# Kernel optimization log

Measured on AMD Instinct MI355X. Metric: run time of the kernel, lower is better.

## Reference

```python
import jax, jax.numpy as jnp
import numpy as np

N, G, MAX_N, E, H = 20000, 200, 100, 320000, 4
F_IN, NHID, NCLS = 128, 128, 10
DQ = 2 * NHID   # pooling-stack input dim = 2*nhid
K1 = 25         # ceil(0.25 * avg_num_nodes)


def _lin(key, fi, fo):
    kw, kb = jax.random.split(key)
    s = 1.0 / np.sqrt(fi)
    return (jax.random.uniform(kw, (fi, fo), jnp.float32, -s, s),
            jax.random.uniform(kb, (fo,), jnp.float32, -s, s))


def setup_inputs():
    key = jax.random.key(0)
    ks = jax.random.split(key, 32)
    x = jax.random.normal(ks[0], (N, F_IN), jnp.float32)
    gid = jax.random.randint(ks[1], (E,), 0, G)
    u = jax.random.randint(ks[2], (E,), 0, MAX_N)
    v = jax.random.randint(ks[3], (E,), 0, MAX_N)
    edge_index = jnp.stack([gid * MAX_N + u, gid * MAX_N + v]).astype(jnp.int32)
    batch = (jnp.arange(N) // MAX_N).astype(jnp.int32)
    d = {}
    d['x'], d['edge_index'], d['batch'] = x, edge_index, batch
    d['W1'], d['b1'] = _lin(ks[4], F_IN, NHID)
    d['W2'], d['b2'] = _lin(ks[5], NHID, NHID)
    d['S0'] = jax.random.normal(ks[6], (1, K1, DQ), jnp.float32) * (1.0 / np.sqrt(DQ))
    d['Wq0'], d['bq0'] = _lin(ks[7], DQ, DQ)
    d['Wk0'], d['bk0'] = _lin(ks[8], DQ, DQ)
    d['Wv0'], d['bv0'] = _lin(ks[9], DQ, DQ)
    d['Wo0'], d['bo0'] = _lin(ks[10], DQ, DQ)
    d['Wq1'], d['bq1'] = _lin(ks[11], DQ, NHID)
    d['Wk1'], d['bk1'] = _lin(ks[12], DQ, NHID)
    d['Wv1'], d['bv1'] = _lin(ks[13], DQ, NHID)
    d['Wo1'], d['bo1'] = _lin(ks[14], NHID, NHID)
    d['S2'] = jax.random.normal(ks[15], (1, 1, NHID), jnp.float32) * (1.0 / np.sqrt(NHID))
    d['Wq2'], d['bq2'] = _lin(ks[16], NHID, NHID)
    d['Wk2'], d['bk2'] = _lin(ks[17], NHID, NHID)
    d['Wv2'], d['bv2'] = _lin(ks[18], NHID, NHID)
    d['Wo2'], d['bo2'] = _lin(ks[19], NHID, NHID)
    d['Wl'], d['bl'] = _lin(ks[20], NHID, NHID)
    d['Wc1'], d['bc1'] = _lin(ks[21], NHID, NHID)
    d['Wc2'], d['bc2'] = _lin(ks[22], NHID, NHID // 2)
    d['Wc3'], d['bc3'] = _lin(ks[23], NHID // 2, NCLS)
    return d


def gcn(h, src, dst, W, b):
    # PyG GCNConv: add self loops, sym-normalize, scatter-add, bias
    h = h @ W
    loop = jnp.arange(N, dtype=src.dtype)
    s = jnp.concatenate([src, loop])
    t = jnp.concatenate([dst, loop])
    deg = jax.ops.segment_sum(jnp.ones(s.shape[0], h.dtype), t, num_segments=N)
    dinv = jax.lax.rsqrt(jnp.maximum(deg, 1.0))
    norm = (dinv[s] * dinv[t])[:, None]
    return jax.ops.segment_sum(h[s] * norm, t, num_segments=N) + b


def to_dense(v, batch):
    counts = jax.ops.segment_sum(jnp.ones(v.shape[0], jnp.int32), batch, num_segments=G)
    start = jnp.cumsum(counts) - counts
    pos = jnp.arange(v.shape[0]) - start[batch]
    dense = jnp.zeros((G, MAX_N, v.shape[1]), v.dtype).at[batch, pos].set(v)
    mask = jnp.zeros((G, MAX_N), bool).at[batch, pos].set(True)
    return dense, mask


def attn_block(Q, K, V, Wo, bo, mask_bias):
    # MAB core with cluster=True: softmax over the QUERY (seed) axis, ln=False
    B, nq, dv = Q.shape
    dh = dv // H
    Qh = Q.reshape(B, nq, H, dh)
    Kh = K.reshape(B, K.shape[1], H, dh)
    Vh = V.reshape(B, V.shape[1], H, dh)
    score = jnp.einsum('bqhd,bkhd->bhqk', Qh, Kh) / jnp.sqrt(jnp.float32(dv))
    if mask_bias is not None:
        score = score + mask_bias[:, None, None, :]
    A = jax.nn.softmax(score, axis=2)  # cluster assignment over seeds
    O = Q + jnp.einsum('bhqk,bkhd->bqhd', A, Vh).reshape(B, nq, dv)
    return O + jax.nn.relu(O @ Wo + bo)


def reference(x, edge_index, batch, W1, b1, W2, b2, S0, Wq0, bq0, Wk0, bk0, Wv0, bv0, Wo0, bo0,
              Wq1, bq1, Wk1, bk1, Wv1, bv1, Wo1, bo1, S2, Wq2, bq2, Wk2, bk2, Wv2, bv2, Wo2, bo2,
              Wl, bl, Wc1, bc1, Wc2, bc2, Wc3, bc3):
    src, dst = edge_index[0], edge_index[1]
    x1 = jax.nn.relu(gcn(x, src, dst, W1, b1))
    x2 = jax.nn.relu(gcn(x1, src, dst, W2, b2))
    p1 = jax.ops.segment_sum(x1, batch, num_segments=G)  # global_add_pool
    p2 = jax.ops.segment_sum(x2, batch, num_segments=G)
    xcat = jnp.concatenate([x1, x2], axis=1)             # [N, 2*nhid]
    dense, mask = to_dense(xcat, batch)
    mask_bias = (1.0 - mask.astype(jnp.float32)) * -1e9
    # --- GMPool_G: PMA with GCNConv for K/V on the node graph ---
    Kd, _ = to_dense(gcn(xcat, src, dst, Wk0, bk0), batch)
    Vd, _ = to_dense(gcn(xcat, src, dst, Wv0, bv0), batch)
    Q0 = jnp.broadcast_to(S0, (G, K1, DQ)) @ Wq0 + bq0
    O0 = attn_block(Q0, Kd, Vd, Wo0, bo0, mask_bias)     # [G, 25, 256]
    # --- SelfAtt (SAB), mask consumed above ---
    Q1 = O0 @ Wq1 + bq1
    K1d = O0 @ Wk1 + bk1
    V1d = O0 @ Wv1 + bv1
    O1 = attn_block(Q1, K1d, V1d, Wo1, bo1, None)        # [G, 25, 128]
    # --- GMPool_I: PMA with 1 seed ---
    Q2 = jnp.broadcast_to(S2, (G, 1, NHID)) @ Wq2 + bq2
    K2d = O1 @ Wk2 + bk2
    V2d = O1 @ Wv2 + bv2
    O2 = attn_block(Q2, K2d, V2d, Wo2, bo2, None)        # [G, 1, 128]
    z = (O2 @ Wl + bl)[:, 0, :]
    z = jax.nn.relu(z @ Wc1 + bc1)                        # dropout = identity at eval
    z = jax.nn.relu(z @ Wc2 + bc2)
    logits = z @ Wc3 + bc3
    return (logits, p1, p2)
```

## Files before the change

### kernel.cpp

```cpp
#include <hip/hip_runtime.h>
#include <hip/hip_bf16.h>
#include <cstdint>
#include <cstddef>

typedef __hip_bfloat16 bf16;
typedef __attribute__((ext_vector_type(8))) short s16x8;
typedef __attribute__((ext_vector_type(4))) float f32x4;

#define MAXN 100
#define HH   4
#define FIN  128
#define KS1  25

static inline int ceil_div(int a, int b){ return (a + b - 1) / b; }

__device__ inline short f2bf(float f){
  unsigned int u = __float_as_uint(f);
  u = (u + 0x7FFF + ((u >> 16) & 1)) >> 16;
  return (short)u;
}
__device__ inline float loadf(const void* s, int i, bool isbf){
  return isbf ? __bfloat162float(((const bf16*)s)[i]) : ((const float*)s)[i];
}
__device__ inline bool block_sniff(const void* x, int tid, int* flagS){
  if (tid < 64){
    unsigned short b = ((const unsigned short*)x)[2 * tid];
    float v = __uint_as_float(((unsigned)b) << 16);
    float a = fabsf(v);
    bool ok = (a >= 6.1e-5f && a <= 16384.f);
    unsigned long long m = __ballot(ok);
    if (tid == 0) *flagS = (__popcll(m) >= 32) ? 1 : 0;
  }
  __syncthreads();
  return *flagS != 0;
}

struct PrepBatch {
  const void* src[40];
  void*       dst[40];
  int         a[40];
  int         b[40];
  int         blk0[41];
  int         ne;
  const void* xptr;
};

__global__ __launch_bounds__(256) void prep_all(PrepBatch pb){
  __shared__ int flagS;
  int tid = threadIdx.x;
  bool isbf = block_sniff(pb.xptr, tid, &flagS);
  int blk = blockIdx.x;
  int t = 0;
  while (t + 1 < pb.ne && pb.blk0[t + 1] <= blk) t++;
  int local = blk - pb.blk0[t];
  const void* s = pb.src[t];
  int bt = pb.b[t];
  if (bt < 0){
    float val = (bt == -2) ? 1.0f : 0.0f;
    int n = pb.a[t];
    float* d = (float*)pb.dst[t];
    int v = local * 256 + tid;
    int base = v * 4;
    if (base + 3 < n) ((float4*)d)[v] = make_float4(val, val, val, val);
    else for (int j = base; j < n && j < base + 4; j++) d[j] = val;
  } else if (bt == 0){
    int n = pb.a[t];
    float* d = (float*)pb.dst[t];
    int v = local * 256 + tid;
    int base = v * 4;
    if (base + 3 < n){
      float4 f;
      if (isbf){
        ushort4 u = ((const ushort4*)s)[v];
        f.x = __uint_as_float(((unsigned)u.x) << 16);
        f.y = __uint_as_float(((unsigned)u.y) << 16);
        f.z = __uint_as_float(((unsigned)u.z) << 16);
        f.w = __uint_as_float(((unsigned)u.w) << 16);
      } else f = ((const float4*)s)[v];
      ((float4*)d)[v] = f;
    } else {
      for (int j = base; j < n && j < base + 4; j++) d[j] = loadf(s, j, isbf);
    }
  } else {
    int K = pb.a[t], Nn = bt, ldt = K + 8;
    short* d = (short*)pb.dst[t];
    int i = local * 256 + tid;
    if (i < K * Nn){
      int n = i / K, k = i - n * K;
      d[(size_t)n * ldt + k] = f2bf(loadf(s, (size_t)k * Nn + n, isbf));
    }
  }
}

__global__ __launch_bounds__(256) void adj_cnt(const int* __restrict__ src, const int* __restrict__ dst,
                                               float* __restrict__ A, int e){
  int i = blockIdx.x * 256 + threadIdx.x;
  if (i >= e) return;
  int s = src[i], d = dst[i];
  int g = d / MAXN;
  int dl = d - g * MAXN;
  int sl = s - (s / MAXN) * MAXN;
  atomicAdd(&A[(size_t)g * (MAXN * MAXN) + dl * MAXN + sl], 1.0f);
}

#define GLDK 136
__global__ __launch_bounds__(512) void gcn_all(
    const void* __restrict__ X,
    const float* __restrict__ Adj,
    const short* __restrict__ W1t, const float* __restrict__ b1,
    const short* __restrict__ W2t, const float* __restrict__ b2,
    short* __restrict__ xaggB,
    float* __restrict__ p1, float* __restrict__ p2)
{
  __shared__ short As[112 * GLDK];
  __shared__ short S1[112 * GLDK];
  __shared__ short S2[128 * GLDK];
  __shared__ short S4[128 * GLDK];
  __shared__ float dinvL[112];
  __shared__ int flagS;
  int g = blockIdx.x;
  int tid = threadIdx.x;
  bool isbf = block_sniff(X, tid, &flagS);
  int wave = tid >> 6, lane = tid & 63;
  int quad = lane >> 4, l16 = lane & 15;
  int gn = wave * 16 + l16;

  for (int i = tid; i < 112 * GLDK / 2; i += 512){ ((int*)As)[i] = 0; ((int*)S1)[i] = 0; }
  for (int i = tid; i < 128 * GLDK / 2; i += 512){ ((int*)S2)[i] = 0; ((int*)S4)[i] = 0; }

  const float* Ag = Adj + (size_t)g * (MAXN * MAXN);
  if (tid < 400){
    int r = tid >> 2, j0 = (tid & 3) * 25;
    const float* row = Ag + r * MAXN + j0;
    float s = 0.f;
#pragma unroll
    for (int j = 0; j < 25; j++) s += row[j];
    s += __shfl_xor(s, 1); s += __shfl_xor(s, 2);
    if ((tid & 3) == 0) dinvL[r] = rsqrtf(1.0f + s);
  }
  __syncthreads();

  for (int i = tid; i < MAXN * MAXN; i += 512){
    int r = i / MAXN, s = i - r * MAXN;
    float v = Ag[i] + (r == s ? 1.0f : 0.0f);
    As[r * GLDK + s] = f2bf(v * dinvL[r] * dinvL[s]);
  }
  for (int i = tid; i < MAXN * 16; i += 512){
    int r = i >> 4, k8 = (i & 15) << 3;
    s16x8 v;
    if (isbf){
      v = *reinterpret_cast<const s16x8*>((const short*)X + (size_t)(g * MAXN + r) * 128 + k8);
    } else {
      const float* ap = (const float*)X + (size_t)(g * MAXN + r) * 128 + k8;
      float4 f0 = *reinterpret_cast<const float4*>(ap);
      float4 f1 = *reinterpret_cast<const float4*>(ap + 4);
      v[0] = f2bf(f0.x); v[1] = f2bf(f0.y); v[2] = f2bf(f0.z); v[3] = f2bf(f0.w);
      v[4] = f2bf(f1.x); v[5] = f2bf(f1.y); v[6] = f2bf(f1.z); v[7] = f2bf(f1.w);
    }
    *reinterpret_cast<s16x8*>(&S1[r * GLDK + k8]) = v;
  }
  __syncthreads();

  f32x4 acc[7];
  auto zacc = [&](){
#pragma unroll
    for (int rt = 0; rt < 7; rt++) acc[rt] = (f32x4){0.f,0.f,0.f,0.f};
  };
  auto passL = [&](const short* Abuf, const short* Bbuf){
#pragma unroll
    for (int kt = 0; kt < 4; kt++){
      int kb = kt * 32 + quad * 8;
      s16x8 bf0 = *reinterpret_cast<const s16x8*>(&Bbuf[gn * GLDK + kb]);
#pragma unroll
      for (int rt = 0; rt < 7; rt++){
        s16x8 a = *reinterpret_cast<const s16x8*>(&Abuf[(rt * 16 + l16) * GLDK + kb]);
        acc[rt] = __builtin_amdgcn_mfma_f32_16x16x32_bf16(a, bf0, acc[rt], 0, 0, 0);
      }
    }
  };
  auto passG = [&](const short* Abuf, const short* __restrict__ Bt){
#pragma unroll
    for (int kt = 0; kt < 4; kt++){
      int kb = kt * 32 + quad * 8;
      s16x8 bf0 = *reinterpret_cast<const s16x8*>(&Bt[(size_t)gn * 136 + kb]);
#pragma unroll
      for (int rt = 0; rt < 7; rt++){
        s16x8 a = *reinterpret_cast<const s16x8*>(&Abuf[(rt * 16 + l16) * GLDK + kb]);
        acc[rt] = __builtin_amdgcn_mfma_f32_16x16x32_bf16(a, bf0, acc[rt], 0, 0, 0);
      }
    }
  };
  auto writeB = [&](short* Bbuf){
#pragma unroll
    for (int rt = 0; rt < 7; rt++){
      short4 o;
      o.x = f2bf(acc[rt][0]); o.y = f2bf(acc[rt][1]);
      o.z = f2bf(acc[rt][2]); o.w = f2bf(acc[rt][3]);
      *reinterpret_cast<short4*>(&Bbuf[gn * GLDK + rt * 16 + quad * 4]) = o;
    }
  };

  float s1sum = 0.f, s2sum = 0.f;
  auto hopEpi = [&](const float* bias, short* AoutA, short* BoutB, float& sum){
    float bv = bias[gn];
#pragma unroll
    for (int rt = 0; rt < 7; rt++){
      float vals[4];
#pragma unroll
      for (int r = 0; r < 4; r++){
        int row = rt * 16 + quad * 4 + r;
        float v = fmaxf(acc[rt][r] + bv, 0.f);
        vals[r] = v;
        if (row < MAXN) sum += v;
      }
      short4 o;
      o.x = f2bf(vals[0]); o.y = f2bf(vals[1]); o.z = f2bf(vals[2]); o.w = f2bf(vals[3]);
      *reinterpret_cast<short4*>(&BoutB[gn * GLDK + rt * 16 + quad * 4]) = o;
      if (AoutA){
        AoutA[(rt * 16 + quad * 4 + 0) * GLDK + gn] = o.x;
        AoutA[(rt * 16 + quad * 4 + 1) * GLDK + gn] = o.y;
        AoutA[(rt * 16 + quad * 4 + 2) * GLDK + gn] = o.z;
        AoutA[(rt * 16 + quad * 4 + 3) * GLDK + gn] = o.w;
      }
    }
  };
  auto xaggEpi = [&](int colbase){
    int col = gn + colbase;
#pragma unroll
    for (int rt = 0; rt < 7; rt++){
#pragma unroll
      for (int r = 0; r < 4; r++){
        int row = rt * 16 + quad * 4 + r;
        if (row < MAXN) xaggB[(size_t)(g * MAXN + row) * 256 + col] = f2bf(acc[rt][r]);
      }
    }
  };

  zacc(); passG(S1, W1t); writeB(S2);
  __syncthreads();
  zacc(); passL(As, S2); hopEpi(b1, S1, S4, s1sum);
  __syncthreads();
  zacc(); passL(As, S4); xaggEpi(0);
  zacc(); passG(S1, W2t); writeB(S2);
  __syncthreads();
  zacc(); passL(As, S2); hopEpi(b2, nullptr, S4, s2sum);
  __syncthreads();
  zacc(); passL(As, S4); xaggEpi(128);

  s1sum += __shfl_xor(s1sum, 16); s1sum += __shfl_xor(s1sum, 32);
  s2sum += __shfl_xor(s2sum, 16); s2sum += __shfl_xor(s2sum, 32);
  if (quad == 0){
    p1[g * 128 + gn] = s1sum;
    p2[g * 128 + gn] = s2sum;
  }
}

__global__ __launch_bounds__(256) void gemm_vds(
    const short* __restrict__ A, int lda,
    const short* __restrict__ Bt, int ldbt,
    const float* __restrict__ bias,
    short* __restrict__ VTg, float* __restrict__ Sg,
    int M, int Nn)
{
  constexpr int K = 256, LDK = K + 8, KU = K / 8, KT = K / 32;
  __shared__ short As[64 * LDK];
  int bm = blockIdx.x * 64, bn = blockIdx.y * 128;
  int tid = threadIdx.x;
  int wave = tid >> 6, lane = tid & 63;
  int quad = lane >> 4, l16 = lane & 15;

  int gn0 = bn + wave * 16 + l16;
  int gn1 = gn0 + 64;
  s16x8 B0[KT], B1[KT];
#pragma unroll
  for (int kt = 0; kt < KT; kt++){
    int kb = kt * 32 + quad * 8;
    s16x8 z;
#pragma unroll
    for (int j = 0; j < 8; j++) z[j] = 0;
    B0[kt] = (gn0 < Nn) ? *reinterpret_cast<const s16x8*>(&Bt[(size_t)gn0 * ldbt + kb]) : z;
    B1[kt] = (gn1 < Nn) ? *reinterpret_cast<const s16x8*>(&Bt[(size_t)gn1 * ldbt + kb]) : z;
  }

  for (int u = tid; u < 64 * KU; u += 256){
    int r = u / KU, k8 = (u - r * KU) << 3;
    int gr = bm + r;
    s16x8 v;
    if (gr < M) v = *reinterpret_cast<const s16x8*>(A + (size_t)gr * lda + k8);
    else {
#pragma unroll
      for (int j = 0; j < 8; j++) v[j] = 0;
    }
    *reinterpret_cast<s16x8*>(&As[r * LDK + k8]) = v;
  }
  __syncthreads();

  f32x4 acc[4][2];
#pragma unroll
  for (int rt = 0; rt < 4; rt++)
#pragma unroll
    for (int g2 = 0; g2 < 2; g2++) acc[rt][g2] = (f32x4){0.f,0.f,0.f,0.f};

  const short* arow = &As[l16 * LDK];
#pragma unroll
  for (int kt = 0; kt < KT; kt++){
    int kb = kt * 32 + quad * 8;
#pragma unroll
    for (int rt = 0; rt < 4; rt++){
      s16x8 a = *reinterpret_cast<const s16x8*>(&arow[rt * 16 * LDK + kb]);
      acc[rt][0] = __builtin_amdgcn_mfma_f32_16x16x32_bf16(a, B0[kt], acc[rt][0], 0, 0, 0);
      acc[rt][1] = __builtin_amdgcn_mfma_f32_16x16x32_bf16(a, B1[kt], acc[rt][1], 0, 0, 0);
    }
  }

#pragma unroll
  for (int g2 = 0; g2 < 2; g2++){
    int gc = (g2 == 0) ? gn0 : gn1;
    if (gc >= Nn) continue;
    float bvv = bias[gc];
#pragma unroll
    for (int rt = 0; rt < 4; rt++){
      int gr0 = bm + rt * 16 + quad * 4;
      if (gc < 256){
        int ga = gr0 / MAXN, gb = (gr0 + 3) / MAXN;
        if (gr0 + 3 < M && ga == gb){
          int node = gr0 - ga * MAXN;
          short4 o;
          o.x = f2bf(acc[rt][g2][0] + bvv); o.y = f2bf(acc[rt][g2][1] + bvv);
          o.z = f2bf(acc[rt][g2][2] + bvv); o.w = f2bf(acc[rt][g2][3] + bvv);
          *reinterpret_cast<short4*>(&VTg[((size_t)ga * 256 + gc) * 128 + node]) = o;
        } else {
#pragma unroll
          for (int r = 0; r < 4; r++){
            int gr = gr0 + r;
            if (gr >= M) continue;
            int gg = gr / MAXN, node = gr - gg * MAXN;
            VTg[((size_t)gg * 256 + gc) * 128 + node] = f2bf(acc[rt][g2][r] + bvv);
          }
        }
      } else {
        int j = gc - 256;
#pragma unroll
        for (int r = 0; r < 4; r++){
          int gr = gr0 + r;
          if (gr >= M) continue;
          int gg = gr / MAXN, node = gr - gg * MAXN;
          Sg[(size_t)gg * 10000 + node * 100 + j] = acc[rt][g2][r] + bvv;
        }
      }
    }
  }
}

__global__ __launch_bounds__(256) void ubar_q0(const float* __restrict__ S0,
    const float* __restrict__ Wq0, const float* __restrict__ bq0,
    const float* __restrict__ Wk0, const float* __restrict__ bk0,
    float* __restrict__ Q0, short* __restrict__ Ubart, float* __restrict__ cvec)
{
  __shared__ float q0s[64];
  int j = blockIdx.x, h = j / 25, q = j - h * 25;
  int tid = threadIdx.x;
  if (tid < 64){
    int c = h * 64 + tid;
    float acc = bq0[c];
    for (int e = 0; e < 256; e++) acc = fmaf(S0[q * 256 + e], Wq0[e * 256 + c], acc);
    q0s[tid] = acc;
    Q0[q * 256 + c] = acc;
  }
  __syncthreads();
  float acc = 0.f;
  const float* wp = &Wk0[(size_t)tid * 256 + h * 64];
#pragma unroll
  for (int d = 0; d < 64; d++) acc = fmaf(wp[d], q0s[d], acc);
  Ubart[(size_t)j * 264 + tid] = f2bf(acc * 0.0625f);
  if (tid == 0){
    float cb = 0.f;
    for (int d = 0; d < 64; d++) cb = fmaf(bk0[h * 64 + d], q0s[d], cb);
    cvec[j] = cb * 0.0625f;
  }
}

struct TailParams {
  const float* Sg;    const short* VTg;   const float* Q0;
  const short* Wo0t;  const float* bo0;
  const short* WQKVt; const float* biasQKV;
  const short* Wo1t;  const float* bo1;
  const float *S2, *Wq2, *bq2, *Wv2, *bv2, *Wo2, *bo2, *Wl, *bl, *Wc1, *bc1, *Wc2, *bc2, *Wc3, *bc3;
  float* out;
};

__global__ __launch_bounds__(512) void tail_all(TailParams P)
{
  __shared__ __align__(16) char pool[138240];
  float* Ssh  = (float*)(pool);
  float* OaF  = (float*)(pool + 40400);
  short* Abf  = (short*)(pool + 66400);
  short* Abf2 = (short*)(pool + 83296);
  float* Ss2  = (float*)(pool + 92000);
  short* Pbf  = (short*)(pool + 102400);
  float* O1F  = (float*)(pool + 102400);
  float* hva  = (float*)(pool + 137216);
  float* hvb  = (float*)(pool + 137728);
  float* QKV = Ssh;
  float* ObF = OaF;
  float* hpart = Ss2;

  int g = blockIdx.x, tid = threadIdx.x;
  int wave = tid >> 6, lane = tid & 63, quad = lane >> 4, l16 = lane & 15;

  const float* sg = P.Sg + (size_t)g * 10000;

  s16x8 vb0[4], vb1[4];
  {
    int cbase = wave * 32;
    const short* vt = P.VTg + (size_t)g * 256 * 128;
#pragma unroll
    for (int kt = 0; kt < 4; kt++){
      int kb = kt * 32 + quad * 8;
      vb0[kt] = *reinterpret_cast<const s16x8*>(&vt[(size_t)(cbase + l16) * 128 + kb]);
      vb1[kt] = *reinterpret_cast<const s16x8*>(&vt[(size_t)(cbase + 16 + l16) * 128 + kb]);
    }
  }

  for (int i = tid; i < 10000; i += 512){
    int k = i / 100, j = i - k * 100;
    Ssh[k * 101 + j] = sg[i];
  }
  for (int i = tid; i < 32 * 264 / 2; i += 512) ((int*)Abf)[i] = 0;
  for (int i = tid; i < 32 * 136 / 2; i += 512) ((int*)Abf2)[i] = 0;
  for (int i = tid; i < 34816 / 4; i += 512) ((int*)Pbf)[i] = 0;
  __syncthreads();

  if (tid < 400){
    int k = tid >> 2, h = tid & 3;
    const float* base = &Ssh[k * 101 + h * 25];
    float v[25];
    float m = -1e30f;
#pragma unroll
    for (int q = 0; q < 25; q++){ v[q] = base[q]; m = fmaxf(m, v[q]); }
    float s = 0.f;
#pragma unroll
    for (int q = 0; q < 25; q++){ float e = __expf(v[q] - m); v[q] = e; s += e; }
    float inv = 1.0f / s;
    short* pb = &Pbf[h * 32 * 136 + k];
#pragma unroll
    for (int q = 0; q < 25; q++) pb[q * 136] = f2bf(v[q] * inv);
  }
  __syncthreads();

  {
    int h = wave >> 1;
    int cbase = wave * 32;
    f32x4 acc[2][2];
#pragma unroll
    for (int rt = 0; rt < 2; rt++){ acc[rt][0] = (f32x4){0.f,0.f,0.f,0.f}; acc[rt][1] = acc[rt][0]; }
#pragma unroll
    for (int kt = 0; kt < 4; kt++){
      int kb = kt * 32 + quad * 8;
#pragma unroll
      for (int rt = 0; rt < 2; rt++){
        s16x8 a = *reinterpret_cast<const s16x8*>(&Pbf[(h * 32 + rt * 16 + l16) * 136 + kb]);
        acc[rt][0] = __builtin_amdgcn_mfma_f32_16x16x32_bf16(a, vb0[kt], acc[rt][0], 0, 0, 0);
        acc[rt][1] = __builtin_amdgcn_mfma_f32_16x16x32_bf16(a, vb1[kt], acc[rt][1], 0, 0, 0);
      }
    }
#pragma unroll
    for (int cg = 0; cg < 2; cg++){
      int c = cbase + cg * 16 + l16;
#pragma unroll
      for (int rt = 0; rt < 2; rt++){
#pragma unroll
        for (int r = 0; r < 4; r++){
          int row = rt * 16 + quad * 4 + r;
          if (row < 25){
            float oa = acc[rt][cg][r] + P.Q0[row * 256 + c];
            OaF[row * 260 + c] = oa;
            Abf[row * 264 + c] = f2bf(oa);
          }
        }
      }
    }
  }
  __syncthreads();

  {
    int c0 = wave * 16 + l16, c1 = c0 + 128;
    s16x8 B0[8], B1[8];
#pragma unroll
    for (int kt = 0; kt < 8; kt++){
      int kb = kt * 32 + quad * 8;
      B0[kt] = *reinterpret_cast<const s16x8*>(&P.Wo0t[(size_t)c0 * 264 + kb]);
      B1[kt] = *reinterpret_cast<const s16x8*>(&P.Wo0t[(size_t)c1 * 264 + kb]);
    }
    f32x4 a0[2], a1[2];
#pragma unroll
    for (int rt = 0; rt < 2; rt++){ a0[rt] = (f32x4){0.f,0.f,0.f,0.f}; a1[rt] = a0[rt]; }
#pragma unroll
    for (int kt = 0; kt < 8; kt++){
      int kb = kt * 32 + quad * 8;
#pragma unroll
      for (int rt = 0; rt < 2; rt++){
        s16x8 a = *reinterpret_cast<const s16x8*>(&Abf[(rt * 16 + l16) * 264 + kb]);
        a0[rt] = __builtin_amdgcn_mfma_f32_16x16x32_bf16(a, B0[kt], a0[rt], 0, 0, 0);
        a1[rt] = __builtin_amdgcn_mfma_f32_16x16x32_bf16(a, B1[kt], a1[rt], 0, 0, 0);
      }
    }
    __syncthreads();
#pragma unroll
    for (int cg = 0; cg < 2; cg++){
      int col = cg ? c1 : c0;
      float bv = P.bo0[col];
#pragma unroll
      for (int rt = 0; rt < 2; rt++){
        f32x4 av = cg ? a1[rt] : a0[rt];
#pragma unroll
        for (int r = 0; r < 4; r++){
          int row = rt * 16 + quad * 4 + r;
          if (row < 25){
            float t = av[r] + bv;
            Abf[row * 264 + col] = f2bf(OaF[row * 260 + col] + fmaxf(t, 0.f));
          }
        }
      }
    }
  }
  __syncthreads();

  {
    int c0 = wave * 16 + l16;
    s16x8 B[3][8];
#pragma unroll
    for (int p2 = 0; p2 < 3; p2++)
#pragma unroll
      for (int kt = 0; kt < 8; kt++){
        int kb = kt * 32 + quad * 8;
        B[p2][kt] = *reinterpret_cast<const s16x8*>(&P.WQKVt[(size_t)(c0 + p2 * 128) * 264 + kb]);
      }
    f32x4 acc[3][2];
#pragma unroll
    for (int p2 = 0; p2 < 3; p2++)
#pragma unroll
      for (int rt = 0; rt < 2; rt++) acc[p2][rt] = (f32x4){0.f,0.f,0.f,0.f};
#pragma unroll
    for (int kt = 0; kt < 8; kt++){
      int kb = kt * 32 + quad * 8;
#pragma unroll
      for (int rt = 0; rt < 2; rt++){
        s16x8 a = *reinterpret_cast<const s16x8*>(&Abf[(rt * 16 + l16) * 264 + kb]);
#pragma unroll
        for (int p2 = 0; p2 < 3; p2++)
          acc[p2][rt] = __builtin_amdgcn_mfma_f32_16x16x32_bf16(a, B[p2][kt], acc[p2][rt], 0, 0, 0);
      }
    }
#pragma unroll
    for (int p2 = 0; p2 < 3; p2++){
      int col = c0 + p2 * 128;
      float bv = P.biasQKV[col];
#pragma unroll
      for (int rt = 0; rt < 2; rt++){
#pragma unroll
        for (int r = 0; r < 4; r++){
          int row = rt * 16 + quad * 4 + r;
          if (row < 25) QKV[row * 388 + col] = acc[p2][rt][r] + bv;
        }
      }
    }
  }
  __syncthreads();

  for (int idx = tid; idx < 2500; idx += 512){
    int h = idx / 625;
    int r = idx - h * 625;
    int q = r / 25, k = r - q * 25;
    const float* qp = &QKV[q * 388 + h * 32];
    const float* kp = &QKV[k * 388 + 128 + h * 32];
    float acc = 0.f;
#pragma unroll
    for (int d = 0; d < 32; d += 4){
      float4 a4 = *reinterpret_cast<const float4*>(&qp[d]);
      float4 b4 = *reinterpret_cast<const float4*>(&kp[d]);
      acc = fmaf(a4.x, b4.x, acc); acc = fmaf(a4.y, b4.y, acc);
      acc = fmaf(a4.z, b4.z, acc); acc = fmaf(a4.w, b4.w, acc);
    }
    Ss2[(h * 25 + q) * 26 + k] = acc * 0.0883883476f;
  }
  __syncthreads();
  if (tid < 100){
    int h = tid / 25, k = tid - h * 25;
    float m = -1e30f;
#pragma unroll
    for (int q = 0; q < 25; q++) m = fmaxf(m, Ss2[(h * 25 + q) * 26 + k]);
    float s = 0.f;
#pragma unroll
    for (int q = 0; q < 25; q++){ float e = __expf(Ss2[(h * 25 + q) * 26 + k] - m); Ss2[(h * 25 + q) * 26 + k] = e; s += e; }
    float inv = 1.0f / s;
#pragma unroll
    for (int q = 0; q < 25; q++) Ss2[(h * 25 + q) * 26 + k] *= inv;
  }
  __syncthreads();

  if (tid < 256){
    int qh = tid >> 7;
    int c = tid & 127, h = c >> 5;
    int q0 = qh * 13, nq = 13 - qh;
    float acc[13] = {};
    for (int k = 0; k < 25; k++){
      float v = QKV[k * 388 + 256 + c];
      for (int j = 0; j < nq; j++)
        acc[j] = fmaf(Ss2[(h * 25 + q0 + j) * 26 + k], v, acc[j]);
    }
    for (int j = 0; j < nq; j++){
      int q = q0 + j;
      float ob = QKV[q * 388 + c] + acc[j];
      ObF[q * 132 + c] = ob;
      Abf2[q * 136 + c] = f2bf(ob);
    }
  }
  __syncthreads();

  {
    int c0 = wave * 16 + l16;
    s16x8 B0[4];
#pragma unroll
    for (int kt = 0; kt < 4; kt++){
      int kb = kt * 32 + quad * 8;
      B0[kt] = *reinterpret_cast<const s16x8*>(&P.Wo1t[(size_t)c0 * 136 + kb]);
    }
    f32x4 a0 = (f32x4){0.f,0.f,0.f,0.f}, a1 = a0;
#pragma unroll
    for (int kt = 0; kt < 4; kt++){
      int kb = kt * 32 + quad * 8;
      s16x8 aA = *reinterpret_cast<const s16x8*>(&Abf2[l16 * 136 + kb]);
      s16x8 aB = *reinterpret_cast<const s16x8*>(&Abf2[(16 + l16) * 136 + kb]);
      a0 = __builtin_amdgcn_mfma_f32_16x16x32_bf16(aA, B0[kt], a0, 0, 0, 0);
      a1 = __builtin_amdgcn_mfma_f32_16x16x32_bf16(aB, B0[kt], a1, 0, 0, 0);
    }
    float bv = P.bo1[c0];
#pragma unroll
    for (int r = 0; r < 4; r++){
      int row0 = quad * 4 + r;
      if (row0 < 25){ float t = a0[r] + bv; O1F[row0 * 132 + c0] = ObF[row0 * 132 + c0] + fmaxf(t, 0.f); }
      int row1 = 16 + quad * 4 + r;
      if (row1 < 25){ float t = a1[r] + bv; O1F[row1 * 132 + c0] = ObF[row1 * 132 + c0] + fmaxf(t, 0.f); }
    }
  }
  __syncthreads();

  if (tid < 128){
    float s = 0.f;
    for (int k = 0; k < 25; k++) s += O1F[k * 132 + tid];
    hva[tid] = s;
  }
  __syncthreads();
  {
    int kh = tid >> 7, c = tid & 127, k0 = kh * 32;
    float s = 0.f;
    for (int k = k0; k < k0 + 32; k++)
      s = fmaf(P.S2[k], P.Wq2[k * 128 + c], fmaf(hva[k], P.Wv2[k * 128 + c], s));
    hpart[kh * 128 + c] = s;
    __syncthreads();
    if (tid < 128) hvb[c] = hpart[c] + hpart[128 + c] + hpart[256 + c] + hpart[384 + c]
                          + P.bq2[c] + 25.f * P.bv2[c];
    __syncthreads();
    s = 0.f;
    for (int k = k0; k < k0 + 32; k++) s = fmaf(hvb[k], P.Wo2[k * 128 + c], s);
    hpart[kh * 128 + c] = s;
    __syncthreads();
    if (tid < 128) hva[c] = hvb[c] + fmaxf(hpart[c] + hpart[128 + c] + hpart[256 + c] + hpart[384 + c] + P.bo2[c], 0.f);
    __syncthreads();
    s = 0.f;
    for (int k = k0; k < k0 + 32; k++) s = fmaf(hva[k], P.Wl[k * 128 + c], s);
    hpart[kh * 128 + c] = s;
    __syncthreads();
    if (tid < 128) hvb[c] = hpart[c] + hpart[128 + c] + hpart[256 + c] + hpart[384 + c] + P.bl[c];
    __syncthreads();
    s = 0.f;
    for (int k = k0; k < k0 + 32; k++) s = fmaf(hvb[k], P.Wc1[k * 128 + c], s);
    hpart[kh * 128 + c] = s;
    __syncthreads();
    if (tid < 128) hva[c] = fmaxf(hpart[c] + hpart[128 + c] + hpart[256 + c] + hpart[384 + c] + P.bc1[c], 0.f);
    __syncthreads();
    {
      int kh2 = tid >> 6, c2 = tid & 63, kk0 = kh2 * 16;
      float s2 = 0.f;
      for (int k = kk0; k < kk0 + 16; k++) s2 = fmaf(hva[k], P.Wc2[k * 64 + c2], s2);
      hpart[kh2 * 64 + c2] = s2;
    }
    __syncthreads();
    if (tid < 64){
      float s2 = hpart[tid] + hpart[64 + tid] + hpart[128 + tid] + hpart[192 + tid]
               + hpart[256 + tid] + hpart[320 + tid] + hpart[384 + tid] + hpart[448 + tid];
      hvb[tid] = fmaxf(s2 + P.bc2[tid], 0.f);
    }
    __syncthreads();
    if (tid < 10){
      float lg = P.bc3[tid];
      for (int k = 0; k < 64; k++) lg = fmaf(hvb[k], P.Wc3[k * 10 + tid], lg);
      P.out[g * 10 + tid] = lg;
    }
  }
}

extern "C" void kernel_launch(void* const* d_in, const int* in_sizes, int n_in,
                              void* d_out, int out_size, void* d_ws, size_t ws_size,
                              hipStream_t stream)
{
  const int*  edge = (const int*)d_in[1];
  const int N = in_sizes[0] / FIN;
  const int E = in_sizes[1] / 2;
  const int G = N / MAXN;
  const int* srcp = edge;
  const int* dstp = edge + E;
  float* out = (float*)d_out;

  float* w = (float*)d_ws;
  size_t off = 0;
  auto alloc = [&](size_t nfl){ nfl = (nfl + 3) & ~(size_t)3; float* p = w + off; off += nfl; return p; };
  auto allocS = [&](size_t nsh)->short*{ size_t nfl = ((nsh + 1) / 2 + 3) & ~(size_t)3; short* p = (short*)(w + off); off += nfl; return p; };

  float* biasVS  = alloc(356);
  float* biasQKV = alloc(384);
  float* cvec = biasVS + 256;

  const int castT[24] = {4,6,7,8,9,10,11,15,23,24,25,26,29,30,31,32,33,34,35,36,37,38,39,40};
  float* wf[41] = {nullptr};
  for (int i = 0; i < 24; i++) wf[castT[i]] = alloc((size_t)in_sizes[castT[i]]);
  wf[13] = biasVS; wf[17] = biasQKV; wf[19] = biasQKV + 128; wf[21] = biasQKV + 256;

  float* Sg  = alloc((size_t)G * 10000);
  short* VTg = allocS((size_t)G * 256 * 128);
  float* Adj = alloc((size_t)G * MAXN * MAXN);
  float* Q0  = alloc(25 * 256);
  short* xaggB = allocS((size_t)N * 256);

  short* W1t   = allocS(128 * 136);
  short* W2t   = allocS(128 * 136);
  short* WVSt  = allocS(356 * 264);
  short* WQKVt = allocS(384 * 264);
  short* Wo0t  = allocS(256 * 264);
  short* Wo1t  = allocS(128 * 136);
  short* Ubart = WVSt + (size_t)256 * 264;
  if (off * sizeof(float) > ws_size) return;

  dim3 blk(256);

  PrepBatch pb; int ne = 0, blks = 0;
  pb.xptr = d_in[0];
  auto addC = [&](const void* s, float* d, int n){
    pb.src[ne]=s; pb.dst[ne]=d; pb.a[ne]=n; pb.b[ne]=0; pb.blk0[ne]=blks;
    blks += ceil_div(ceil_div(n, 4), 256); ne++; };
  auto addW = [&](const void* s, short* d, int K, int Nn){
    pb.src[ne]=s; pb.dst[ne]=d; pb.a[ne]=K; pb.b[ne]=Nn; pb.blk0[ne]=blks;
    blks += ceil_div(K * Nn, 256); ne++; };
  auto addF = [&](void* d, int n, int mode){
    pb.src[ne]=nullptr; pb.dst[ne]=d; pb.a[ne]=n; pb.b[ne]=mode; pb.blk0[ne]=blks;
    blks += ceil_div(ceil_div(n, 4), 256); ne++; };
  for (int i = 0; i < 24; i++){ int t = castT[i]; addC(d_in[t], wf[t], in_sizes[t]); }
  addC(d_in[13], biasVS, 256);
  addC(d_in[17], biasQKV, 128); addC(d_in[19], biasQKV + 128, 128); addC(d_in[21], biasQKV + 256, 128);
  addW(d_in[3],  W1t, 128, 128);             addW(d_in[5],  W2t, 128, 128);
  addW(d_in[12], WVSt, 256, 256);            addW(d_in[16], WQKVt, 256, 128);
  addW(d_in[18], WQKVt + 128*264, 256, 128); addW(d_in[20], WQKVt + 256*264, 256, 128);
  addW(d_in[14], Wo0t, 256, 256);            addW(d_in[22], Wo1t, 128, 128);
  addF(Adj, G * MAXN * MAXN, -1);
  pb.blk0[ne] = blks; pb.ne = ne;
  prep_all<<<dim3(blks), blk, 0, stream>>>(pb);

  adj_cnt<<<ceil_div(E, 256), blk, 0, stream>>>(srcp, dstp, Adj, E);

  gcn_all<<<dim3(G), dim3(512), 0, stream>>>(d_in[0], Adj, W1t, wf[4], W2t, wf[6],
                                             xaggB, out + 2000, out + 27600);

  ubar_q0<<<dim3(100), blk, 0, stream>>>(wf[7], wf[8], wf[9], wf[10], wf[11], Q0, Ubart, cvec);

  {
    dim3 grid(ceil_div(N, 64), 3);
    gemm_vds<<<grid, blk, 0, stream>>>(xaggB, 256, WVSt, 264, biasVS, VTg, Sg, N, 356);
  }

  TailParams tp;
  tp.Sg = Sg; tp.VTg = VTg; tp.Q0 = Q0;
  tp.Wo0t = Wo0t; tp.bo0 = wf[15];
  tp.WQKVt = WQKVt; tp.biasQKV = biasQKV;
  tp.Wo1t = Wo1t; tp.bo1 = wf[23];
  tp.S2 = wf[24]; tp.Wq2 = wf[25]; tp.bq2 = wf[26]; tp.Wv2 = wf[29]; tp.bv2 = wf[30];
  tp.Wo2 = wf[31]; tp.bo2 = wf[32]; tp.Wl = wf[33]; tp.bl = wf[34];
  tp.Wc1 = wf[35]; tp.bc1 = wf[36]; tp.Wc2 = wf[37]; tp.bc2 = wf[38];
  tp.Wc3 = wf[39]; tp.bc3 = wf[40];
  tp.out = out;
  tail_all<<<dim3(G), dim3(512), 0, stream>>>(tp);
}
```

Before: 262.1 us.

## Fuse V/score projection GEMM into per-graph tail kernel via swizzled LDS

Removes the separate gemm_vds launch. Each tail_all block now loads its graph's 100 aggregated node rows into XOR-swizzled LDS and computes the V projection and attention scores with MFMA in place. This avoids the global round-trip of VTg and Sg plus one kernel launch. In exchange the LDS footprint grows to about 160KB, and the GEMM work is spread over only 200 blocks instead of a wider grid.

```diff
diff --git a/kernel.cpp b/kernel.cpp
--- a/kernel.cpp
+++ b/kernel.cpp
@@ -255,103 +255,6 @@
   }
 }
 
-__global__ __launch_bounds__(256) void gemm_vds(
-    const short* __restrict__ A, int lda,
-    const short* __restrict__ Bt, int ldbt,
-    const float* __restrict__ bias,
-    short* __restrict__ VTg, float* __restrict__ Sg,
-    int M, int Nn)
-{
-  constexpr int K = 256, LDK = K + 8, KU = K / 8, KT = K / 32;
-  __shared__ short As[64 * LDK];
-  int bm = blockIdx.x * 64, bn = blockIdx.y * 128;
-  int tid = threadIdx.x;
-  int wave = tid >> 6, lane = tid & 63;
-  int quad = lane >> 4, l16 = lane & 15;
-
-  int gn0 = bn + wave * 16 + l16;
-  int gn1 = gn0 + 64;
-  s16x8 B0[KT], B1[KT];
-#pragma unroll
-  for (int kt = 0; kt < KT; kt++){
-    int kb = kt * 32 + quad * 8;
-    s16x8 z;
-#pragma unroll
-    for (int j = 0; j < 8; j++) z[j] = 0;
-    B0[kt] = (gn0 < Nn) ? *reinterpret_cast<const s16x8*>(&Bt[(size_t)gn0 * ldbt + kb]) : z;
-    B1[kt] = (gn1 < Nn) ? *reinterpret_cast<const s16x8*>(&Bt[(size_t)gn1 * ldbt + kb]) : z;
-  }
-
-  for (int u = tid; u < 64 * KU; u += 256){
-    int r = u / KU, k8 = (u - r * KU) << 3;
-    int gr = bm + r;
-    s16x8 v;
-    if (gr < M) v = *reinterpret_cast<const s16x8*>(A + (size_t)gr * lda + k8);
-    else {
-#pragma unroll
-      for (int j = 0; j < 8; j++) v[j] = 0;
-    }
-    *reinterpret_cast<s16x8*>(&As[r * LDK + k8]) = v;
-  }
-  __syncthreads();
-
-  f32x4 acc[4][2];
-#pragma unroll
-  for (int rt = 0; rt < 4; rt++)
-#pragma unroll
-    for (int g2 = 0; g2 < 2; g2++) acc[rt][g2] = (f32x4){0.f,0.f,0.f,0.f};
-
-  const short* arow = &As[l16 * LDK];
-#pragma unroll
-  for (int kt = 0; kt < KT; kt++){
-    int kb = kt * 32 + quad * 8;
-#pragma unroll
-    for (int rt = 0; rt < 4; rt++){
-      s16x8 a = *reinterpret_cast<const s16x8*>(&arow[rt * 16 * LDK + kb]);
-      acc[rt][0] = __builtin_amdgcn_mfma_f32_16x16x32_bf16(a, B0[kt], acc[rt][0], 0, 0, 0);
-      acc[rt][1] = __builtin_amdgcn_mfma_f32_16x16x32_bf16(a, B1[kt], acc[rt][1], 0, 0, 0);
-    }
-  }
-
-#pragma unroll
-  for (int g2 = 0; g2 < 2; g2++){
-    int gc = (g2 == 0) ? gn0 : gn1;
-    if (gc >= Nn) continue;
-    float bvv = bias[gc];
-#pragma unroll
-    for (int rt = 0; rt < 4; rt++){
-      int gr0 = bm + rt * 16 + quad * 4;
-      if (gc < 256){
-        int ga = gr0 / MAXN, gb = (gr0 + 3) / MAXN;
-        if (gr0 + 3 < M && ga == gb){
-          int node = gr0 - ga * MAXN;
-          short4 o;
-          o.x = f2bf(acc[rt][g2][0] + bvv); o.y = f2bf(acc[rt][g2][1] + bvv);
-          o.z = f2bf(acc[rt][g2][2] + bvv); o.w = f2bf(acc[rt][g2][3] + bvv);
-          *reinterpret_cast<short4*>(&VTg[((size_t)ga * 256 + gc) * 128 + node]) = o;
-        } else {
-#pragma unroll
-          for (int r = 0; r < 4; r++){
-            int gr = gr0 + r;
-            if (gr >= M) continue;
-            int gg = gr / MAXN, node = gr - gg * MAXN;
-            VTg[((size_t)gg * 256 + gc) * 128 + node] = f2bf(acc[rt][g2][r] + bvv);
-          }
-        }
-      } else {
-        int j = gc - 256;
-#pragma unroll
-        for (int r = 0; r < 4; r++){
-          int gr = gr0 + r;
-          if (gr >= M) continue;
-          int gg = gr / MAXN, node = gr - gg * MAXN;
-          Sg[(size_t)gg * 10000 + node * 100 + j] = acc[rt][g2][r] + bvv;
-        }
-      }
-    }
-  }
-}
-
 __global__ __launch_bounds__(256) void ubar_q0(const float* __restrict__ S0,
     const float* __restrict__ Wq0, const float* __restrict__ bq0,
     const float* __restrict__ Wk0, const float* __restrict__ bk0,
@@ -381,7 +284,11 @@
 }
 
 struct TailParams {
-  const float* Sg;    const short* VTg;   const float* Q0;
+  const short* xaggB;
+  const short* Wv0t;
+  const short* Ubart;
+  const float* biasVS;
+  const float* Q0;
   const short* Wo0t;  const float* bo0;
   const short* WQKVt; const float* biasQKV;
   const short* Wo1t;  const float* bo1;
@@ -391,49 +298,121 @@
 
 __global__ __launch_bounds__(512) void tail_all(TailParams P)
 {
-  __shared__ __align__(16) char pool[138240];
-  float* Ssh  = (float*)(pool);
-  float* OaF  = (float*)(pool + 40400);
-  short* Abf  = (short*)(pool + 66400);
-  short* Abf2 = (short*)(pool + 83296);
-  float* Ss2  = (float*)(pool + 92000);
-  short* Pbf  = (short*)(pool + 102400);
-  float* O1F  = (float*)(pool + 102400);
-  float* hva  = (float*)(pool + 137216);
-  float* hvb  = (float*)(pool + 137728);
-  float* QKV = Ssh;
-  float* ObF = OaF;
-  float* hpart = Ss2;
+  __shared__ __align__(16) char pool[162880];
+  char*  R1   = pool;
+  char*  R2   = pool + 57344;
+  char*  R3   = pool + 97344;
+  float* Ssh  = (float*)R2;
+  short* Pbf  = (short*)R1;
+  short* Abf  = (short*)(R1 + 34816);
+  float* hva  = (float*)(R1 + 51712);
+  float* hvb  = (float*)(R1 + 52224);
+  float* O1F  = (float*)R1;
+  float* OaF  = (float*)R2;
+  float* ObF  = (float*)R2;
+  short* Abf2 = (short*)(R2 + 26000);
+  float* QKV  = (float*)R3;
+  float* Ss2  = (float*)(R3 + 38800);
+  float* hpart= (float*)(R3 + 38800);
 
   int g = blockIdx.x, tid = threadIdx.x;
   int wave = tid >> 6, lane = tid & 63, quad = lane >> 4, l16 = lane & 15;
 
-  const float* sg = P.Sg + (size_t)g * 10000;
-
-  s16x8 vb0[4], vb1[4];
   {
-    int cbase = wave * 32;
-    const short* vt = P.VTg + (size_t)g * 256 * 128;
-#pragma unroll
-    for (int kt = 0; kt < 4; kt++){
-      int kb = kt * 32 + quad * 8;
-      vb0[kt] = *reinterpret_cast<const s16x8*>(&vt[(size_t)(cbase + l16) * 128 + kb]);
-      vb1[kt] = *reinterpret_cast<const s16x8*>(&vt[(size_t)(cbase + 16 + l16) * 128 + kb]);
-    }
-  }
-
-  for (int i = tid; i < 10000; i += 512){
-    int k = i / 100, j = i - k * 100;
-    Ssh[k * 101 + j] = sg[i];
-  }
-  for (int i = tid; i < 32 * 264 / 2; i += 512) ((int*)Abf)[i] = 0;
-  for (int i = tid; i < 32 * 136 / 2; i += 512) ((int*)Abf2)[i] = 0;
-  for (int i = tid; i < 34816 / 4; i += 512) ((int*)Pbf)[i] = 0;
+    const short* xa = P.xaggB + (size_t)g * MAXN * 256;
+    for (int i = tid; i < 3200; i += 512){
+      int r = i >> 5, ch = i & 31;
+      s16x8 v = *reinterpret_cast<const s16x8*>(xa + r * 256 + ch * 8);
+      int b = (r * 512 + ch * 16) ^ ((r & 7) << 4);
+      *reinterpret_cast<s16x8*>(R1 + b) = v;
+    }
+    s16x8 z; 
+#pragma unroll
+    for (int j = 0; j < 8; j++) z[j] = 0;
+    if (tid < 384){
+      int r = 100 + (tid >> 5), ch = tid & 31;
+      int b = (r * 512 + ch * 16) ^ ((r & 7) << 4);
+      *reinterpret_cast<s16x8*>(R1 + b) = z;
+    }
+    {
+      int c = tid >> 1, slot = tid & 1;
+      int b = (c * 256 + 224 + slot * 16) ^ ((c & 7) << 4);
+      *reinterpret_cast<s16x8*>(R3 + b) = z;
+    }
+  }
+  __syncthreads();
+
+  {
+#pragma unroll
+    for (int cg = 0; cg < 2; cg++){
+      int c = wave * 32 + cg * 16 + l16;
+      const short* bw = P.Wv0t + (size_t)c * 264;
+      s16x8 B[8];
+#pragma unroll
+      for (int kt = 0; kt < 8; kt++) B[kt] = *reinterpret_cast<const s16x8*>(bw + kt * 32 + quad * 8);
+      f32x4 acc[7];
+#pragma unroll
+      for (int rt = 0; rt < 7; rt++) acc[rt] = (f32x4){0.f,0.f,0.f,0.f};
+#pragma unroll
+      for (int kt = 0; kt < 8; kt++){
+        int kb = kt * 32 + quad * 8;
+#pragma unroll
+        for (int rt = 0; rt < 7; rt++){
+          int row = rt * 16 + l16;
+          int ab = (row * 512 + kb * 2) ^ ((row & 7) << 4);
+          s16x8 a = *reinterpret_cast<const s16x8*>(R1 + ab);
+          acc[rt] = __builtin_amdgcn_mfma_f32_16x16x32_bf16(a, B[kt], acc[rt], 0, 0, 0);
+        }
+      }
+      float bv = P.biasVS[c];
+#pragma unroll
+      for (int rt = 0; rt < 7; rt++){
+        int node0 = rt * 16 + quad * 4;
+        short4 o;
+        o.x = f2bf(acc[rt][0] + bv); o.y = f2bf(acc[rt][1] + bv);
+        o.z = f2bf(acc[rt][2] + bv); o.w = f2bf(acc[rt][3] + bv);
+        int b = (c * 256 + node0 * 2) ^ ((c & 7) << 4);
+        *reinterpret_cast<short4*>(R3 + b) = o;
+      }
+    }
+    if (wave < 7){
+      int j = wave * 16 + l16;
+      const short* bw = P.Ubart + (size_t)j * 264;
+      s16x8 B[8];
+#pragma unroll
+      for (int kt = 0; kt < 8; kt++) B[kt] = *reinterpret_cast<const s16x8*>(bw + kt * 32 + quad * 8);
+      f32x4 acc[7];
+#pragma unroll
+      for (int rt = 0; rt < 7; rt++) acc[rt] = (f32x4){0.f,0.f,0.f,0.f};
+#pragma unroll
+      for (int kt = 0; kt < 8; kt++){
+        int kb = kt * 32 + quad * 8;
+#pragma unroll
+        for (int rt = 0; rt < 7; rt++){
+          int row = rt * 16 + l16;
+          int ab = (row * 512 + kb * 2) ^ ((row & 7) << 4);
+          s16x8 a = *reinterpret_cast<const s16x8*>(R1 + ab);
+          acc[rt] = __builtin_amdgcn_mfma_f32_16x16x32_bf16(a, B[kt], acc[rt], 0, 0, 0);
+        }
+      }
+      if (j < 100){
+        float cv = P.biasVS[256 + j];
+#pragma unroll
+        for (int rt = 0; rt < 7; rt++){
+#pragma unroll
+          for (int r = 0; r < 4; r++){
+            int node = rt * 16 + quad * 4 + r;
+            if (node < MAXN) Ssh[node * 100 + j] = acc[rt][r] + cv;
+          }
+        }
+      }
+    }
+  }
   __syncthreads();
 
   if (tid < 400){
     int k = tid >> 2, h = tid & 3;
-    const float* base = &Ssh[k * 101 + h * 25];
+    const float* base = &Ssh[k * 100 + h * 25];
     float v[25];
     float m = -1e30f;
 #pragma unroll
@@ -445,6 +424,12 @@
     short* pb = &Pbf[h * 32 * 136 + k];
 #pragma unroll
     for (int q = 0; q < 25; q++) pb[q * 136] = f2bf(v[q] * inv);
+  } else {
+    for (int idx = tid - 400; idx < 1400; idx += 112){
+      int r = idx / 14, c = idx - r * 14;
+      int h = r / 25, q = r - h * 25;
+      ((int*)Pbf)[(h * 32 + q) * 68 + 50 + c] = 0;
+    }
   }
   __syncthreads();
 
@@ -457,11 +442,16 @@
 #pragma unroll
     for (int kt = 0; kt < 4; kt++){
       int kb = kt * 32 + quad * 8;
+      int c0 = cbase + l16, c1 = cbase + 16 + l16;
+      int b0 = (c0 * 256 + kb * 2) ^ ((c0 & 7) << 4);
+      int b1 = (c1 * 256 + kb * 2) ^ ((c1 & 7) << 4);
+      s16x8 vb0 = *reinterpret_cast<const s16x8*>(R3 + b0);
+      s16x8 vb1 = *reinterpret_cast<const s16x8*>(R3 + b1);
 #pragma unroll
       for (int rt = 0; rt < 2; rt++){
         s16x8 a = *reinterpret_cast<const s16x8*>(&Pbf[(h * 32 + rt * 16 + l16) * 136 + kb]);
-        acc[rt][0] = __builtin_amdgcn_mfma_f32_16x16x32_bf16(a, vb0[kt], acc[rt][0], 0, 0, 0);
-        acc[rt][1] = __builtin_amdgcn_mfma_f32_16x16x32_bf16(a, vb1[kt], acc[rt][1], 0, 0, 0);
+        acc[rt][0] = __builtin_amdgcn_mfma_f32_16x16x32_bf16(a, vb0, acc[rt][0], 0, 0, 0);
+        acc[rt][1] = __builtin_amdgcn_mfma_f32_16x16x32_bf16(a, vb1, acc[rt][1], 0, 0, 0);
       }
     }
 #pragma unroll
@@ -727,8 +717,6 @@
   for (int i = 0; i < 24; i++) wf[castT[i]] = alloc((size_t)in_sizes[castT[i]]);
   wf[13] = biasVS; wf[17] = biasQKV; wf[19] = biasQKV + 128; wf[21] = biasQKV + 256;
 
-  float* Sg  = alloc((size_t)G * 10000);
-  short* VTg = allocS((size_t)G * 256 * 128);
   float* Adj = alloc((size_t)G * MAXN * MAXN);
   float* Q0  = alloc(25 * 256);
   short* xaggB = allocS((size_t)N * 256);
@@ -773,13 +761,9 @@
 
   ubar_q0<<<dim3(100), blk, 0, stream>>>(wf[7], wf[8], wf[9], wf[10], wf[11], Q0, Ubart, cvec);
 
-  {
-    dim3 grid(ceil_div(N, 64), 3);
-    gemm_vds<<<grid, blk, 0, stream>>>(xaggB, 256, WVSt, 264, biasVS, VTg, Sg, N, 356);
-  }
-
   TailParams tp;
-  tp.Sg = Sg; tp.VTg = VTg; tp.Q0 = Q0;
+  tp.xaggB = xaggB; tp.Wv0t = WVSt; tp.Ubart = Ubart; tp.biasVS = biasVS;
+  tp.Q0 = Q0;
   tp.Wo0t = Wo0t; tp.bo0 = wf[15];
   tp.WQKVt = WQKVt; tp.biasQKV = biasQKV;
   tp.Wo1t = Wo1t; tp.bo1 = wf[23];
```

Result: faster. 241.6 us (-7.8%).
